# Kernel optimization log

Measured on AMD Instinct MI355X. Metric: run time of the kernel, lower is better.

## Reference

```python
import jax, jax.numpy as jnp
import numpy as np
import itertools

N_SUBSETS = 4
TAU = 0.1


def setup_inputs() -> dict:
    key = jax.random.key(0)
    k1, k2, k3 = jax.random.split(key, 3)
    # scale projections so exp(sim/tau) stays numerically sane (module assumes small/normalized projections)
    projections = jax.random.normal(k1, (8192, 128), dtype=jnp.float32) * 0.05
    xrecon = jax.random.normal(k2, (8192, 784), dtype=jnp.float32)
    recon_label = jax.random.normal(k3, (8192, 784), dtype=jnp.float32)
    return {"projections": projections, "xrecon": xrecon, "recon_label": recon_label}


def _joint_loss(projections, xrecon, recon_label):
    # reconstruction MSE
    recon_loss = jnp.mean(jnp.square(xrecon - recon_label))

    # ---- XNegloss (SimCLR-style with n_subsets positives per group) ----
    N, D = projections.shape
    sim = (projections @ projections.T) / TAU  # [N, N] dot similarity
    gid = jnp.arange(N) // N_SUBSETS
    pos_mask = gid[:, None] == gid[None, :]  # same-group entries are positives
    exp_sim = jnp.exp(sim)
    # original code drops positive entries exactly equal to 1 (positives[positives != 1])
    pos_sum = jnp.sum(jnp.where(pos_mask & (sim != 1.0), exp_sim, 0.0), axis=-1)
    neg_sum = jnp.sum(jnp.where(pos_mask, 0.0, exp_sim), axis=-1)
    closs = jnp.mean(-jnp.log(pos_sum / (pos_sum + neg_sum)))

    # ---- distance loss: MSE over all subset pairs within each group ----
    combi = np.array(list(itertools.combinations(range(N_SUBSETS), 2)))
    left, right = combi[:, 0], combi[:, 1]
    P = projections.reshape(N // N_SUBSETS, N_SUBSETS, D)
    # per-group mean over (pairs, D) then mean over groups == global mean (equal counts)
    dist_loss = jnp.mean(jnp.square(P[:, left] - P[:, right]))

    loss = recon_loss + closs + dist_loss
    return loss, closs, recon_loss, dist_loss


def reference(projections, xrecon, recon_label):
    return _joint_loss(projections, xrecon, recon_label)
```

## Files before the change

### kernel.cpp

```cpp
#include <hip/hip_runtime.h>
#include <hip/hip_bf16.h>
#include <stdint.h>

typedef __bf16 bf16x8 __attribute__((ext_vector_type(8)));
typedef float  f32x4  __attribute__((ext_vector_type(4)));

#define NROWS   8192
#define DIMK    128
#define NGROUPS 2048
#define RECON_N 6422528
#define SIM_BLOCKS   512
#define RECON_BLOCKS 1568
#define GROUP_BLOCKS (NGROUPS / 4)
#define FUSED_BLOCKS (SIM_BLOCKS + RECON_BLOCKS + GROUP_BLOCKS)
#define CLOSS_BLOCKS 32

#define WS_SP     0
#define WS_G      65536
#define WS_E      73728
#define WS_RPART  81920
#define WS_DPART  83488
#define WS_CPART  84000
#define WS_PB     84032

__device__ __forceinline__ void async16(const void* g, void* l) {
    __builtin_amdgcn_global_load_lds(
        (const __attribute__((address_space(1))) void*)g,
        (__attribute__((address_space(3))) void*)l, 16, 0, 0);
}

__device__ __forceinline__ unsigned short f2bf(float f) {
    union { __hip_bfloat16 h; unsigned short u; } v;
    v.h = __float2bfloat16(f);
    return v.u;
}

__global__ __launch_bounds__(256) void convert_kernel(const float4* __restrict__ P,
                                                      uint2* __restrict__ out) {
    int idx = blockIdx.x * 256 + threadIdx.x;
    float4 a = P[idx];
    uint2 r;
    r.x = (uint32_t)f2bf(a.x) | ((uint32_t)f2bf(a.y) << 16);
    r.y = (uint32_t)f2bf(a.z) | ((uint32_t)f2bf(a.w) << 16);
    out[idx] = r;
}

__global__ __launch_bounds__(256, 2) void fused_kernel(
        const unsigned short* __restrict__ Pb,
        const float* __restrict__ Pf,
        const float4* __restrict__ X,
        const float4* __restrict__ Y,
        float* __restrict__ ws) {
    const int bx = blockIdx.x;
    const int wave = threadIdx.x >> 6, lane = threadIdx.x & 63;

    int role, idx;
    if (bx < 2560) {
        int r5 = bx % 5, c5 = bx / 5;
        if (r5 == 0)      { role = 0; idx = c5; }
        else if (r5 == 4) { role = 2; idx = c5; }
        else              { role = 1; idx = c5 * 3 + (r5 - 1); }
    } else {
        role = 1; idx = 1536 + (bx - 2560);
    }

    if (role == 0) {
        __shared__ unsigned short tile[128 * 128];
        __shared__ float sred[2][2][64];
        float* Sp = ws + WS_SP;
        const int wr = wave >> 1, wc = wave & 1;
        const int rowBase = (idx >> 3) * 128;
        const int colBase = (idx & 7) * 1024;

        {
            const char* g = (const char*)(Pb + (size_t)rowBase * DIMK);
#pragma unroll
            for (int i = 0; i < 8; ++i) {
                int seg = i * 4 + wave;
                async16(g + seg * 1024 + lane * 16, (char*)tile + seg * 1024);
            }
        }
        __syncthreads();

        bf16x8 Af[4][4];
        {
            int m = lane & 15, kq = lane >> 4;
#pragma unroll
            for (int i = 0; i < 4; ++i) {
                const unsigned short* rowp = tile + (wr * 64 + i * 16 + m) * 128 + kq * 8;
#pragma unroll
                for (int kk = 0; kk < 4; ++kk)
                    Af[i][kk] = *(const bf16x8*)(rowp + kk * 32);
            }
        }
        __syncthreads();

        float rowAcc[4][4];
#pragma unroll
        for (int i = 0; i < 4; ++i)
#pragma unroll
            for (int r = 0; r < 4; ++r) rowAcc[i][r] = 0.f;

        for (int t = 0; t < 8; ++t) {
            {
                const char* g = (const char*)(Pb + (size_t)(colBase + t * 128) * DIMK);
#pragma unroll
                for (int i = 0; i < 8; ++i) {
                    int seg = i * 4 + wave;
                    async16(g + seg * 1024 + lane * 16, (char*)tile + seg * 1024);
                }
            }
            __syncthreads();

            f32x4 acc[4][4];
#pragma unroll
            for (int i = 0; i < 4; ++i)
#pragma unroll
                for (int j = 0; j < 4; ++j) acc[i][j] = (f32x4){0.f, 0.f, 0.f, 0.f};

            int n = lane & 15, kq = lane >> 4;
#pragma unroll
            for (int kk = 0; kk < 4; ++kk) {
                bf16x8 Bf[4];
#pragma unroll
                for (int j = 0; j < 4; ++j)
                    Bf[j] = *(const bf16x8*)(tile + (wc * 64 + j * 16 + n) * 128 + kq * 8 + kk * 32);
#pragma unroll
                for (int i = 0; i < 4; ++i)
#pragma unroll
                    for (int j = 0; j < 4; ++j)
                        acc[i][j] = __builtin_amdgcn_mfma_f32_16x16x32_bf16(
                            Af[i][kk], Bf[j], acc[i][j], 0, 0, 0);
            }
#pragma unroll
            for (int i = 0; i < 4; ++i)
#pragma unroll
                for (int j = 0; j < 4; ++j)
#pragma unroll
                    for (int r = 0; r < 4; ++r)
                        rowAcc[i][r] += __expf(acc[i][j][r] * 10.0f);
            __syncthreads();
        }

#pragma unroll
        for (int i = 0; i < 4; ++i)
#pragma unroll
            for (int r = 0; r < 4; ++r) {
                float sv = rowAcc[i][r];
                sv += __shfl_xor(sv, 1, 64);
                sv += __shfl_xor(sv, 2, 64);
                sv += __shfl_xor(sv, 4, 64);
                sv += __shfl_xor(sv, 8, 64);
                rowAcc[i][r] = sv;
            }
        if ((lane & 15) == 0) {
            int c = lane >> 4;
#pragma unroll
            for (int i = 0; i < 4; ++i)
#pragma unroll
                for (int r = 0; r < 4; ++r)
                    sred[wc][wr][i * 16 + c * 4 + r] = rowAcc[i][r];
        }
        __syncthreads();
        if (wc == 0) {
            float v = sred[0][wr][lane] + sred[1][wr][lane];
            Sp[(size_t)(idx & 7) * NROWS + rowBase + wr * 64 + lane] = v;
        }
    } else if (role == 1) {
        __shared__ float red[4];
        int base = idx * 1024 + threadIdx.x;
        float4 a0 = X[base], b0 = Y[base];
        float4 a1 = X[base + 256], b1 = Y[base + 256];
        float4 a2 = X[base + 512], b2 = Y[base + 512];
        float4 a3 = X[base + 768], b3 = Y[base + 768];
        float s = 0.f, d;
        d = a0.x - b0.x; s += d * d;  d = a0.y - b0.y; s += d * d;
        d = a0.z - b0.z; s += d * d;  d = a0.w - b0.w; s += d * d;
        d = a1.x - b1.x; s += d * d;  d = a1.y - b1.y; s += d * d;
        d = a1.z - b1.z; s += d * d;  d = a1.w - b1.w; s += d * d;
        d = a2.x - b2.x; s += d * d;  d = a2.y - b2.y; s += d * d;
        d = a2.z - b2.z; s += d * d;  d = a2.w - b2.w; s += d * d;
        d = a3.x - b3.x; s += d * d;  d = a3.y - b3.y; s += d * d;
        d = a3.z - b3.z; s += d * d;  d = a3.w - b3.w; s += d * d;
#pragma unroll
        for (int mm = 1; mm < 64; mm <<= 1) s += __shfl_xor(s, mm, 64);
        if (lane == 0) red[wave] = s;
        __syncthreads();
        if (threadIdx.x == 0)
            ws[WS_RPART + idx] = red[0] + red[1] + red[2] + red[3];
    } else {
        __shared__ float dred[4];
        float* G = ws + WS_G;
        float* E = ws + WS_E;
        int g = idx * 4 + wave;
        const float* base = Pf + (size_t)g * 4 * DIMK;
        float v[4][2];
#pragma unroll
        for (int r = 0; r < 4; ++r) {
            v[r][0] = base[r * DIMK + lane];
            v[r][1] = base[r * DIMK + 64 + lane];
        }
        float dmat[4][4];
#pragma unroll
        for (int r = 0; r < 4; ++r)
#pragma unroll
            for (int s2 = r; s2 < 4; ++s2) {
                float p = v[r][0] * v[s2][0] + v[r][1] * v[s2][1];
#pragma unroll
                for (int mm = 1; mm < 64; mm <<= 1) p += __shfl_xor(p, mm, 64);
                dmat[r][s2] = p; dmat[s2][r] = p;
            }
        if (lane == 0) {
            float distp = 0.f;
#pragma unroll
            for (int r = 0; r < 4; ++r)
#pragma unroll
                for (int s2 = r + 1; s2 < 4; ++s2)
                    distp += dmat[r][r] + dmat[s2][s2] - 2.f * dmat[r][s2];
            dred[wave] = distp;
#pragma unroll
            for (int r = 0; r < 4; ++r) {
                float Gs = 0.f, Es = 0.f;
#pragma unroll
                for (int s2 = 0; s2 < 4; ++s2) {
                    float sim = dmat[r][s2] * 10.0f;
                    float e = __expf(sim);
                    Gs += e;
                    if (sim == 1.0f) Es += e;
                }
                G[g * 4 + r] = Gs;
                E[g * 4 + r] = Es;
            }
        }
        __syncthreads();
        if (threadIdx.x == 0)
            ws[WS_DPART + idx] = dred[0] + dred[1] + dred[2] + dred[3];
    }
}

__global__ __launch_bounds__(256) void closs_kernel(const float* __restrict__ ws,
                                                    float* __restrict__ cpart) {
    __shared__ float red[4];
    const float* Sp = ws + WS_SP;
    const float* G  = ws + WS_G;
    const float* E  = ws + WS_E;
    int r = blockIdx.x * 256 + threadIdx.x;
    float Sv = 0.f;
#pragma unroll
    for (int q = 0; q < 8; ++q) Sv += Sp[q * NROWS + r];
    float c = __logf(Sv - E[r]) - __logf(G[r] - E[r]);
#pragma unroll
    for (int m = 1; m < 64; m <<= 1) c += __shfl_xor(c, m, 64);
    int wave = threadIdx.x >> 6, lane = threadIdx.x & 63;
    if (lane == 0) red[wave] = c;
    __syncthreads();
    if (threadIdx.x == 0)
        cpart[blockIdx.x] = red[0] + red[1] + red[2] + red[3];
}

__global__ __launch_bounds__(256) void combine_kernel(const float* __restrict__ ws,
                                                      float* __restrict__ out) {
    __shared__ float redc[4], redr[4], redd[4];
    float cs = 0.f, rs = 0.f, ds = 0.f;
    for (int i = threadIdx.x; i < CLOSS_BLOCKS; i += 256) cs += ws[WS_CPART + i];
    for (int i = threadIdx.x; i < RECON_BLOCKS; i += 256) rs += ws[WS_RPART + i];
    for (int i = threadIdx.x; i < GROUP_BLOCKS; i += 256) ds += ws[WS_DPART + i];
#pragma unroll
    for (int m = 1; m < 64; m <<= 1) {
        cs += __shfl_xor(cs, m, 64);
        rs += __shfl_xor(rs, m, 64);
        ds += __shfl_xor(ds, m, 64);
    }
    int wave = threadIdx.x >> 6, lane = threadIdx.x & 63;
    if (lane == 0) { redc[wave] = cs; redr[wave] = rs; redd[wave] = ds; }
    __syncthreads();
    if (threadIdx.x == 0) {
        float closs = (redc[0] + redc[1] + redc[2] + redc[3]) / (float)NROWS;
        float recon = (redr[0] + redr[1] + redr[2] + redr[3]) / (float)RECON_N;
        float dist  = (redd[0] + redd[1] + redd[2] + redd[3]) / (float)(NGROUPS * 6 * DIMK);
        out[0] = recon + closs + dist;
        out[1] = closs;
        out[2] = recon;
        out[3] = dist;
    }
}

extern "C" void kernel_launch(void* const* d_in, const int* in_sizes, int n_in,
                              void* d_out, int out_size, void* d_ws, size_t ws_size,
                              hipStream_t stream) {
    const float* P  = (const float*)d_in[0];
    const float4* X = (const float4*)d_in[1];
    const float4* Y = (const float4*)d_in[2];
    float* out = (float*)d_out;
    float* w = (float*)d_ws;
    unsigned short* Pb = (unsigned short*)(w + WS_PB);

    convert_kernel<<<NROWS * DIMK / 4 / 256, 256, 0, stream>>>((const float4*)P, (uint2*)Pb);
    fused_kernel<<<FUSED_BLOCKS, 256, 0, stream>>>(Pb, P, X, Y, w);
    closs_kernel<<<CLOSS_BLOCKS, 256, 0, stream>>>(w, w + WS_CPART);
    combine_kernel<<<1, 256, 0, stream>>>(w, out);
}
```

Measured before the change: 134.2 us.

## Restructure pipeline: fuse convert into prep, split sim kernel with swizzled LDS and atomics

Moves the bf16 conversion into a prep kernel alongside the recon and group-distance work, and runs the similarity GEMM as its own kernel. That kernel uses a 1024-block grid over 512-column strips with an XOR-rotated LDS layout meant to avoid bank conflicts. Row sums are accumulated with atomicAdd into a memset buffer, which removes the separate closs kernel, and a single 1024-thread finalize does the reductions. The trade-off is an extra memset launch, atomic contention, and no longer overlapping the memory-bound recon work with the compute-bound GEMM.

```diff
diff --git a/kernel.cpp b/kernel.cpp
--- a/kernel.cpp
+++ b/kernel.cpp
@@ -9,19 +9,18 @@
 #define DIMK    128
 #define NGROUPS 2048
 #define RECON_N 6422528
-#define SIM_BLOCKS   512
 #define RECON_BLOCKS 1568
-#define GROUP_BLOCKS (NGROUPS / 4)
-#define FUSED_BLOCKS (SIM_BLOCKS + RECON_BLOCKS + GROUP_BLOCKS)
-#define CLOSS_BLOCKS 32
-
-#define WS_SP     0
-#define WS_G      65536
-#define WS_E      73728
-#define WS_RPART  81920
-#define WS_DPART  83488
-#define WS_CPART  84000
-#define WS_PB     84032
+#define GROUP_BLOCKS 512
+#define CONV_BLOCKS  1024
+#define PREP_BLOCKS (RECON_BLOCKS + GROUP_BLOCKS + CONV_BLOCKS)
+#define SIM_BLOCKS   1024
+
+#define WS_S      0
+#define WS_G      8192
+#define WS_E      16384
+#define WS_RPART  24576
+#define WS_DPART  26144
+#define WS_PB     26656
 
 __device__ __forceinline__ void async16(const void* g, void* l) {
     __builtin_amdgcn_global_load_lds(
@@ -35,141 +34,19 @@
     return v.u;
 }
 
-__global__ __launch_bounds__(256) void convert_kernel(const float4* __restrict__ P,
-                                                      uint2* __restrict__ out) {
-    int idx = blockIdx.x * 256 + threadIdx.x;
-    float4 a = P[idx];
-    uint2 r;
-    r.x = (uint32_t)f2bf(a.x) | ((uint32_t)f2bf(a.y) << 16);
-    r.y = (uint32_t)f2bf(a.z) | ((uint32_t)f2bf(a.w) << 16);
-    out[idx] = r;
-}
-
-__global__ __launch_bounds__(256, 2) void fused_kernel(
-        const unsigned short* __restrict__ Pb,
+__global__ __launch_bounds__(256) void prep_kernel(
         const float* __restrict__ Pf,
         const float4* __restrict__ X,
         const float4* __restrict__ Y,
+        uint2* __restrict__ Pb,
         float* __restrict__ ws) {
     const int bx = blockIdx.x;
     const int wave = threadIdx.x >> 6, lane = threadIdx.x & 63;
 
-    int role, idx;
-    if (bx < 2560) {
-        int r5 = bx % 5, c5 = bx / 5;
-        if (r5 == 0)      { role = 0; idx = c5; }
-        else if (r5 == 4) { role = 2; idx = c5; }
-        else              { role = 1; idx = c5 * 3 + (r5 - 1); }
-    } else {
-        role = 1; idx = 1536 + (bx - 2560);
-    }
-
-    if (role == 0) {
-        __shared__ unsigned short tile[128 * 128];
-        __shared__ float sred[2][2][64];
-        float* Sp = ws + WS_SP;
-        const int wr = wave >> 1, wc = wave & 1;
-        const int rowBase = (idx >> 3) * 128;
-        const int colBase = (idx & 7) * 1024;
-
-        {
-            const char* g = (const char*)(Pb + (size_t)rowBase * DIMK);
-#pragma unroll
-            for (int i = 0; i < 8; ++i) {
-                int seg = i * 4 + wave;
-                async16(g + seg * 1024 + lane * 16, (char*)tile + seg * 1024);
-            }
-        }
-        __syncthreads();
-
-        bf16x8 Af[4][4];
-        {
-            int m = lane & 15, kq = lane >> 4;
-#pragma unroll
-            for (int i = 0; i < 4; ++i) {
-                const unsigned short* rowp = tile + (wr * 64 + i * 16 + m) * 128 + kq * 8;
-#pragma unroll
-                for (int kk = 0; kk < 4; ++kk)
-                    Af[i][kk] = *(const bf16x8*)(rowp + kk * 32);
-            }
-        }
-        __syncthreads();
-
-        float rowAcc[4][4];
-#pragma unroll
-        for (int i = 0; i < 4; ++i)
-#pragma unroll
-            for (int r = 0; r < 4; ++r) rowAcc[i][r] = 0.f;
-
-        for (int t = 0; t < 8; ++t) {
-            {
-                const char* g = (const char*)(Pb + (size_t)(colBase + t * 128) * DIMK);
-#pragma unroll
-                for (int i = 0; i < 8; ++i) {
-                    int seg = i * 4 + wave;
-                    async16(g + seg * 1024 + lane * 16, (char*)tile + seg * 1024);
-                }
-            }
-            __syncthreads();
-
-            f32x4 acc[4][4];
-#pragma unroll
-            for (int i = 0; i < 4; ++i)
-#pragma unroll
-                for (int j = 0; j < 4; ++j) acc[i][j] = (f32x4){0.f, 0.f, 0.f, 0.f};
-
-            int n = lane & 15, kq = lane >> 4;
-#pragma unroll
-            for (int kk = 0; kk < 4; ++kk) {
-                bf16x8 Bf[4];
-#pragma unroll
-                for (int j = 0; j < 4; ++j)
-                    Bf[j] = *(const bf16x8*)(tile + (wc * 64 + j * 16 + n) * 128 + kq * 8 + kk * 32);
-#pragma unroll
-                for (int i = 0; i < 4; ++i)
-#pragma unroll
-                    for (int j = 0; j < 4; ++j)
-                        acc[i][j] = __builtin_amdgcn_mfma_f32_16x16x32_bf16(
-                            Af[i][kk], Bf[j], acc[i][j], 0, 0, 0);
-            }
-#pragma unroll
-            for (int i = 0; i < 4; ++i)
-#pragma unroll
-                for (int j = 0; j < 4; ++j)
-#pragma unroll
-                    for (int r = 0; r < 4; ++r)
-                        rowAcc[i][r] += __expf(acc[i][j][r] * 10.0f);
-            __syncthreads();
-        }
-
-#pragma unroll
-        for (int i = 0; i < 4; ++i)
-#pragma unroll
-            for (int r = 0; r < 4; ++r) {
-                float sv = rowAcc[i][r];
-                sv += __shfl_xor(sv, 1, 64);
-                sv += __shfl_xor(sv, 2, 64);
-                sv += __shfl_xor(sv, 4, 64);
-                sv += __shfl_xor(sv, 8, 64);
-                rowAcc[i][r] = sv;
-            }
-        if ((lane & 15) == 0) {
-            int c = lane >> 4;
-#pragma unroll
-            for (int i = 0; i < 4; ++i)
-#pragma unroll
-                for (int r = 0; r < 4; ++r)
-                    sred[wc][wr][i * 16 + c * 4 + r] = rowAcc[i][r];
-        }
-        __syncthreads();
-        if (wc == 0) {
-            float v = sred[0][wr][lane] + sred[1][wr][lane];
-            Sp[(size_t)(idx & 7) * NROWS + rowBase + wr * 64 + lane] = v;
-        }
-    } else if (role == 1) {
+    if (bx < RECON_BLOCKS) {
         __shared__ float red[4];
-        int base = idx * 1024 + threadIdx.x;
-        float4 a0 = X[base], b0 = Y[base];
+        int base = bx * 1024 + threadIdx.x;
+        float4 a0 = X[base],       b0 = Y[base];
         float4 a1 = X[base + 256], b1 = Y[base + 256];
         float4 a2 = X[base + 512], b2 = Y[base + 512];
         float4 a3 = X[base + 768], b3 = Y[base + 768];
@@ -187,12 +64,13 @@
         if (lane == 0) red[wave] = s;
         __syncthreads();
         if (threadIdx.x == 0)
-            ws[WS_RPART + idx] = red[0] + red[1] + red[2] + red[3];
-    } else {
+            ws[WS_RPART + bx] = red[0] + red[1] + red[2] + red[3];
+    } else if (bx < RECON_BLOCKS + GROUP_BLOCKS) {
         __shared__ float dred[4];
+        int gb = bx - RECON_BLOCKS;
         float* G = ws + WS_G;
         float* E = ws + WS_E;
-        int g = idx * 4 + wave;
+        int g = gb * 4 + wave;
         const float* base = Pf + (size_t)g * 4 * DIMK;
         float v[4][2];
 #pragma unroll
@@ -234,50 +112,161 @@
         }
         __syncthreads();
         if (threadIdx.x == 0)
-            ws[WS_DPART + idx] = dred[0] + dred[1] + dred[2] + dred[3];
-    }
-}
-
-__global__ __launch_bounds__(256) void closs_kernel(const float* __restrict__ ws,
-                                                    float* __restrict__ cpart) {
-    __shared__ float red[4];
-    const float* Sp = ws + WS_SP;
-    const float* G  = ws + WS_G;
-    const float* E  = ws + WS_E;
-    int r = blockIdx.x * 256 + threadIdx.x;
-    float Sv = 0.f;
-#pragma unroll
-    for (int q = 0; q < 8; ++q) Sv += Sp[q * NROWS + r];
-    float c = __logf(Sv - E[r]) - __logf(G[r] - E[r]);
-#pragma unroll
-    for (int m = 1; m < 64; m <<= 1) c += __shfl_xor(c, m, 64);
+            ws[WS_DPART + gb] = dred[0] + dred[1] + dred[2] + dred[3];
+    } else {
+        int cb = bx - (RECON_BLOCKS + GROUP_BLOCKS);
+        int idx = cb * 256 + threadIdx.x;
+        float4 a = ((const float4*)Pf)[idx];
+        uint2 r;
+        r.x = (uint32_t)f2bf(a.x) | ((uint32_t)f2bf(a.y) << 16);
+        r.y = (uint32_t)f2bf(a.z) | ((uint32_t)f2bf(a.w) << 16);
+        Pb[idx] = r;
+    }
+}
+
+__global__ __launch_bounds__(256, 3) void sim_kernel(
+        const unsigned short* __restrict__ Pb,
+        float* __restrict__ S) {
+    __shared__ unsigned short tile[128 * 128];
+    const int bx = blockIdx.x;
+    const int wave = threadIdx.x >> 6, lane = threadIdx.x & 63;
+    const int wr = wave >> 1, wc = wave & 1;
+    const int rowBase = (bx >> 4) * 128;
+    const int colBase = (bx & 15) * 512;
+    const int m = lane & 15, kq = lane >> 4;
+
+    int srcOff[8];
+#pragma unroll
+    for (int i = 0; i < 8; ++i) {
+        int seg = i * 4 + wave;
+        int chunk = seg * 64 + lane;
+        int r = chunk >> 4, qp = chunk & 15;
+        int q = (qp - r) & 15;
+        srcOff[i] = r * 256 + q * 16;
+    }
+
+    {
+        const char* g = (const char*)(Pb + (size_t)rowBase * DIMK);
+#pragma unroll
+        for (int i = 0; i < 8; ++i) {
+            int seg = i * 4 + wave;
+            async16(g + srcOff[i], (char*)tile + seg * 1024 + lane * 16);
+        }
+    }
+    __syncthreads();
+
+    bf16x8 Af[4][4];
+#pragma unroll
+    for (int i = 0; i < 4; ++i) {
+        int rl = wr * 64 + i * 16 + m;
+#pragma unroll
+        for (int kk = 0; kk < 4; ++kk)
+            Af[i][kk] = *(const bf16x8*)((const char*)tile + rl * 256 +
+                                         (((kq + kk * 4 + rl) & 15) << 4));
+    }
+    __syncthreads();
+
+    float rowAcc[4][4];
+#pragma unroll
+    for (int i = 0; i < 4; ++i)
+#pragma unroll
+        for (int r = 0; r < 4; ++r) rowAcc[i][r] = 0.f;
+
+    for (int t = 0; t < 4; ++t) {
+        {
+            const char* g = (const char*)(Pb + (size_t)(colBase + t * 128) * DIMK);
+#pragma unroll
+            for (int i = 0; i < 8; ++i) {
+                int seg = i * 4 + wave;
+                async16(g + srcOff[i], (char*)tile + seg * 1024 + lane * 16);
+            }
+        }
+        __syncthreads();
+
+        f32x4 acc[4][4];
+#pragma unroll
+        for (int i = 0; i < 4; ++i)
+#pragma unroll
+            for (int j = 0; j < 4; ++j) acc[i][j] = (f32x4){0.f, 0.f, 0.f, 0.f};
+
+#pragma unroll
+        for (int kk = 0; kk < 4; ++kk) {
+            bf16x8 Bf[4];
+#pragma unroll
+            for (int j = 0; j < 4; ++j) {
+                int rl = wc * 64 + j * 16 + m;
+                Bf[j] = *(const bf16x8*)((const char*)tile + rl * 256 +
+                                         (((kq + kk * 4 + rl) & 15) << 4));
+            }
+#pragma unroll
+            for (int i = 0; i < 4; ++i)
+#pragma unroll
+                for (int j = 0; j < 4; ++j)
+                    acc[i][j] = __builtin_amdgcn_mfma_f32_16x16x32_bf16(
+                        Af[i][kk], Bf[j], acc[i][j], 0, 0, 0);
+        }
+#pragma unroll
+        for (int i = 0; i < 4; ++i)
+#pragma unroll
+            for (int j = 0; j < 4; ++j)
+#pragma unroll
+                for (int r = 0; r < 4; ++r)
+                    rowAcc[i][r] += __expf(acc[i][j][r] * 10.0f);
+        __syncthreads();
+    }
+
+#pragma unroll
+    for (int i = 0; i < 4; ++i)
+#pragma unroll
+        for (int r = 0; r < 4; ++r) {
+            float sv = rowAcc[i][r];
+            sv += __shfl_xor(sv, 1, 64);
+            sv += __shfl_xor(sv, 2, 64);
+            sv += __shfl_xor(sv, 4, 64);
+            sv += __shfl_xor(sv, 8, 64);
+            rowAcc[i][r] = sv;
+        }
+    if ((lane & 15) == 0) {
+        int c = lane >> 4;
+#pragma unroll
+        for (int i = 0; i < 4; ++i)
+#pragma unroll
+            for (int r = 0; r < 4; ++r)
+                atomicAdd(&S[rowBase + wr * 64 + i * 16 + c * 4 + r], rowAcc[i][r]);
+    }
+}
+
+__global__ __launch_bounds__(1024) void finalize_kernel(const float* __restrict__ ws,
+                                                        float* __restrict__ out) {
+    __shared__ float redc[16], redr[16], redd[16];
+    const float* S = ws + WS_S;
+    const float* G = ws + WS_G;
+    const float* E = ws + WS_E;
+
+    float c = 0.f;
+    for (int r = threadIdx.x; r < NROWS; r += 1024)
+        c += __logf(S[r] - E[r]) - __logf(G[r] - E[r]);
+    float rs = 0.f;
+    for (int i = threadIdx.x; i < RECON_BLOCKS; i += 1024) rs += ws[WS_RPART + i];
+    float ds = 0.f;
+    for (int i = threadIdx.x; i < GROUP_BLOCKS; i += 1024) ds += ws[WS_DPART + i];
+
+#pragma unroll
+    for (int mm = 1; mm < 64; mm <<= 1) {
+        c  += __shfl_xor(c,  mm, 64);
+        rs += __shfl_xor(rs, mm, 64);
+        ds += __shfl_xor(ds, mm, 64);
+    }
     int wave = threadIdx.x >> 6, lane = threadIdx.x & 63;
-    if (lane == 0) red[wave] = c;
-    __syncthreads();
-    if (threadIdx.x == 0)
-        cpart[blockIdx.x] = red[0] + red[1] + red[2] + red[3];
-}
-
-__global__ __launch_bounds__(256) void combine_kernel(const float* __restrict__ ws,
-                                                      float* __restrict__ out) {
-    __shared__ float redc[4], redr[4], redd[4];
-    float cs = 0.f, rs = 0.f, ds = 0.f;
-    for (int i = threadIdx.x; i < CLOSS_BLOCKS; i += 256) cs += ws[WS_CPART + i];
-    for (int i = threadIdx.x; i < RECON_BLOCKS; i += 256) rs += ws[WS_RPART + i];
-    for (int i = threadIdx.x; i < GROUP_BLOCKS; i += 256) ds += ws[WS_DPART + i];
-#pragma unroll
-    for (int m = 1; m < 64; m <<= 1) {
-        cs += __shfl_xor(cs, m, 64);
-        rs += __shfl_xor(rs, m, 64);
-        ds += __shfl_xor(ds, m, 64);
-    }
-    int wave = threadIdx.x >> 6, lane = threadIdx.x & 63;
-    if (lane == 0) { redc[wave] = cs; redr[wave] = rs; redd[wave] = ds; }
+    if (lane == 0) { redc[wave] = c; redr[wave] = rs; redd[wave] = ds; }
     __syncthreads();
     if (threadIdx.x == 0) {
-        float closs = (redc[0] + redc[1] + redc[2] + redc[3]) / (float)NROWS;
-        float recon = (redr[0] + redr[1] + redr[2] + redr[3]) / (float)RECON_N;
-        float dist  = (redd[0] + redd[1] + redd[2] + redd[3]) / (float)(NGROUPS * 6 * DIMK);
+        float cs = 0.f, rss = 0.f, dss = 0.f;
+#pragma unroll
+        for (int i = 0; i < 16; ++i) { cs += redc[i]; rss += redr[i]; dss += redd[i]; }
+        float closs = cs / (float)NROWS;
+        float recon = rss / (float)RECON_N;
+        float dist  = dss / (float)(NGROUPS * 6 * DIMK);
         out[0] = recon + closs + dist;
         out[1] = closs;
         out[2] = recon;
@@ -295,8 +284,8 @@
     float* w = (float*)d_ws;
     unsigned short* Pb = (unsigned short*)(w + WS_PB);
 
-    convert_kernel<<<NROWS * DIMK / 4 / 256, 256, 0, stream>>>((const float4*)P, (uint2*)Pb);
-    fused_kernel<<<FUSED_BLOCKS, 256, 0, stream>>>(Pb, P, X, Y, w);
-    closs_kernel<<<CLOSS_BLOCKS, 256, 0, stream>>>(w, w + WS_CPART);
-    combine_kernel<<<1, 256, 0, stream>>>(w, out);
-}
+    hipMemsetAsync(w + WS_S, 0, NROWS * sizeof(float), stream);
+    prep_kernel<<<PREP_BLOCKS, 256, 0, stream>>>(P, X, Y, (uint2*)Pb, w);
+    sim_kernel<<<SIM_BLOCKS, 256, 0, stream>>>(Pb, w + WS_S);
+    finalize_kernel<<<1, 1024, 0, stream>>>(w, out);
+}
```

Result: slower. 138.0 us (+2.8%).
